# Performance work log

Hardware: AMD Instinct MI355X
Metric: run time of the kernel (lower is better)

The kernel has to match this reference:

```python
import jax, jax.numpy as jnp
import numpy as np

NUM_HEADS = 12


def setup_inputs() -> dict:
    key = jax.random.key(0)
    ks = jax.random.split(key, 5)
    B, N, D = 8, 1024, 768
    x = jax.random.normal(ks[0], (B, N, D), dtype=jnp.float32)
    w_qkv = jax.random.normal(ks[1], (D, 3 * D), dtype=jnp.float32) * (D ** -0.5)
    b_qkv = jax.random.normal(ks[2], (3 * D,), dtype=jnp.float32) * 0.02
    w_proj = jax.random.normal(ks[3], (D, D), dtype=jnp.float32) * (D ** -0.5)
    b_proj = jax.random.normal(ks[4], (D,), dtype=jnp.float32) * 0.02
    return {"x": x, "w_qkv": w_qkv, "b_qkv": b_qkv, "w_proj": w_proj, "b_proj": b_proj}


def reference(x, w_qkv, b_qkv, w_proj, b_proj):
    B, N, D = x.shape
    H = NUM_HEADS
    hd = D // H
    scale = hd ** -0.5
    qkv = x @ w_qkv + b_qkv                      # [B, N, 3D]
    qkv = qkv.reshape(B, N, 3, H, hd)
    q, k, v = jnp.moveaxis(qkv, 2, 0)            # each [B, N, H, hd]
    # scores: [B, H, N, N]
    scores = jnp.einsum("bqhd,bkhd->bhqk", q, k) * scale
    attn = jax.nn.softmax(scores, axis=-1)
    a = jnp.einsum("bhqk,bkhd->bqhd", attn, v)   # [B, N, H, hd]
    a = a.reshape(B, N, D)
    return a @ w_proj + b_proj
```

## Files before the change

### kernel.cpp

```cpp
#include <hip/hip_runtime.h>

#define B_ 8
#define N_ 1024
#define D_ 768
#define H_ 12
#define HD 64
#define M_ (B_*N_)

typedef short short8 __attribute__((ext_vector_type(8)));
typedef float f32x4 __attribute__((ext_vector_type(4)));
typedef float f32x16 __attribute__((ext_vector_type(16)));
typedef int int4v __attribute__((ext_vector_type(4)));

__device__ __forceinline__ unsigned short f2bf(float f) {
    union { float f; unsigned int u; } c; c.f = f;
    unsigned int u = c.u;
    unsigned int r = (u + 0x7fffu + ((u >> 16) & 1u)) >> 16;
    return (unsigned short)r;
}

__device__ __forceinline__ float exp2_hw(float x) {
    float r;
    asm("v_exp_f32 %0, %1" : "=v"(r) : "v"(x));
    return r;
}

__device__ __forceinline__ unsigned int cvtpk_bf16(float a, float b) {
    unsigned int r;
    asm("v_cvt_pk_bf16_f32 %0, %1, %2" : "=v"(r) : "v"(a), "v"(b));
    return r;
}

#define PLSWAP(a, b) asm volatile("v_permlane32_swap_b32 %0, %1" : "+&v"(a), "+&v"(b))

__device__ __forceinline__ short8 pack4(unsigned int a, unsigned int b,
                                        unsigned int c, unsigned int d) {
    union { int4v i; short8 s; } u;
    u.i = (int4v){(int)a, (int)b, (int)c, (int)d};
    return u.s;
}

__device__ __forceinline__ void gload16(const void* g, void* l) {
    __builtin_amdgcn_global_load_lds(
        (const __attribute__((address_space(1))) unsigned int*)g,
        (__attribute__((address_space(3))) unsigned int*)l, 16, 0, 0);
}


__global__ __launch_bounds__(256) void prep_kernel(
    const float* __restrict__ x, const float* __restrict__ wqkv,
    const float* __restrict__ wproj,
    unsigned short* __restrict__ xb, unsigned short* __restrict__ wqkvT,
    unsigned short* __restrict__ wprojT)
{
    int bid = blockIdx.x, tid = threadIdx.x;
    if (bid < 6144) {
        int i = bid * 256 + tid;
        float4 v = reinterpret_cast<const float4*>(x)[i];
        ushort4 o;
        o.x = f2bf(v.x); o.y = f2bf(v.y); o.z = f2bf(v.z); o.w = f2bf(v.w);
        reinterpret_cast<ushort4*>(xb)[i] = o;
    } else if (bid < 6144 + 6912) {
        int i = (bid - 6144) * 256 + tid;
        int r = i / 2304, c = i - r * 2304;
        wqkvT[c * 768 + r] = f2bf(wqkv[i]);
    } else {
        int i = (bid - 13056) * 256 + tid;
        int r = i / 768, c = i - r * 768;
        wprojT[c * 768 + r] = f2bf(wproj[i]);
    }
}


template<int MODE>
__global__ __launch_bounds__(256) void gemm_kernel(
    const unsigned short* __restrict__ A,
    const unsigned short* __restrict__ Bt,
    const float* __restrict__ bias,
    float* __restrict__ outf,
    unsigned short* __restrict__ qo,
    unsigned short* __restrict__ ko,
    unsigned short* __restrict__ vo,
    int Ndim, int K)
{
    __shared__ alignas(16) unsigned short As[3 * 4096];
    __shared__ alignas(16) unsigned short Bs[3 * 4096];

    int tid = threadIdx.x;
    int lane = tid & 63, w = tid >> 6;
    int wr = w >> 1, wc = w & 1;

    int nbx = Ndim >> 7;
    int nwg = gridDim.x;
    int cpx = nwg >> 3;
    int sbid = (blockIdx.x & 7) * cpx + (blockIdx.x >> 3);
    int bx = sbid % nbx, by = sbid / nbx;
    int m0 = by * 128, n0 = bx * 128;

    int lr = lane & 15, lk8 = (lane >> 4) * 8;
    int org = (lane >> 4) * 4;

    int srow = tid >> 2;
    int selem = (tid & 3) * 8;
    const unsigned short* gA = A + (size_t)(m0 + srow) * K + selem;
    const unsigned short* gB = Bt + (size_t)(n0 + srow) * K + selem;

    f32x4 acc[4][4] = {};

#define GSTAGE(buf, k0)                                                    \
    do {                                                                   \
        gload16(gA + (k0), As + (buf) * 4096 + w * 512);                   \
        gload16(gA + (size_t)64 * K + (k0), As + (buf) * 4096 + 2048 + w * 512);\
        gload16(gB + (k0), Bs + (buf) * 4096 + w * 512);                   \
        gload16(gB + (size_t)64 * K + (k0), Bs + (buf) * 4096 + 2048 + w * 512);\
    } while (0)

    GSTAGE(0, 0);
    GSTAGE(1, 32);
    asm volatile("s_waitcnt vmcnt(4)" ::: "memory");
    __builtin_amdgcn_s_barrier();
    __builtin_amdgcn_sched_barrier(0);

    int KT = K >> 5;
    int cur = 0;
    for (int kt = 0; kt < KT; ++kt) {
        int sb = cur + 2; if (sb >= 3) sb -= 3;
        if (kt + 2 < KT) GSTAGE(sb, (kt + 2) * 32);

        const unsigned short* Ab = As + cur * 4096;
        const unsigned short* Bb = Bs + cur * 4096;
        short8 af[4], bf[4];
        #pragma unroll
        for (int mi = 0; mi < 4; mi++)
            af[mi] = *reinterpret_cast<const short8*>(&Ab[(wr * 64 + mi * 16 + lr) * 32 + lk8]);
        #pragma unroll
        for (int ni = 0; ni < 4; ni++)
            bf[ni] = *reinterpret_cast<const short8*>(&Bb[(wc * 64 + ni * 16 + lr) * 32 + lk8]);
        #pragma unroll
        for (int mi = 0; mi < 4; mi++)
            #pragma unroll
            for (int ni = 0; ni < 4; ni++)
                acc[mi][ni] = (MODE == 1)
                    ? __builtin_amdgcn_mfma_f32_16x16x32_bf16(bf[ni], af[mi], acc[mi][ni], 0, 0, 0)
                    : __builtin_amdgcn_mfma_f32_16x16x32_bf16(af[mi], bf[ni], acc[mi][ni], 0, 0, 0);

        if (kt + 1 < KT) {
            if (kt + 2 < KT)
                asm volatile("s_waitcnt vmcnt(4)" ::: "memory");
            else
                asm volatile("s_waitcnt vmcnt(0)" ::: "memory");
            __builtin_amdgcn_s_barrier();
            __builtin_amdgcn_sched_barrier(0);
            cur = (cur == 2) ? 0 : cur + 1;
        }
    }
#undef GSTAGE

    if (MODE == 1) {
        int m = m0 + wr * 64 + lr;
        #pragma unroll
        for (int mi = 0; mi < 4; mi++) {
            int row = m + mi * 16;
            #pragma unroll
            for (int ni = 0; ni < 4; ni++) {
                int col = n0 + wc * 64 + ni * 16 + org;
                float4 bv = *reinterpret_cast<const float4*>(&bias[col]);
                float4 o;
                o.x = acc[mi][ni][0] + bv.x;
                o.y = acc[mi][ni][1] + bv.y;
                o.z = acc[mi][ni][2] + bv.z;
                o.w = acc[mi][ni][3] + bv.w;
                *reinterpret_cast<float4*>(&outf[(size_t)row * Ndim + col]) = o;
            }
        }
        return;
    }

    if (n0 >= 1536) {
        #pragma unroll
        for (int mi = 0; mi < 4; mi++) {
            int nn0g = m0 + wr * 64 + mi * 16 + org;
            int b = nn0g >> 10, nn = nn0g & 1023;
            #pragma unroll
            for (int ni = 0; ni < 4; ni++) {
                int colg = n0 + wc * 64 + ni * 16 + lr;
                int rem = colg - 1536;
                int h = rem >> 6, dd = rem & 63;
                float bv = bias[colg];
                unsigned long long u = 0;
                #pragma unroll
                for (int r = 0; r < 4; r++)
                    u |= (unsigned long long)f2bf(acc[mi][ni][r] + bv) << (16 * r);
                *reinterpret_cast<unsigned long long*>(
                    vo + ((size_t)(b * H_ + h) * HD + dd) * N_ + nn) = u;
            }
        }
    } else {
        int which = n0 / 768;
        unsigned short* dst = (which == 0) ? qo : ko;
        float fold = (which == 0) ? 0.125f * 1.44269504088896f : 1.0f;
        #pragma unroll
        for (int mi = 0; mi < 4; mi++) {
            #pragma unroll
            for (int ni = 0; ni < 4; ni++) {
                int col = n0 + wc * 64 + ni * 16 + lr;
                int rem = col - which * 768;
                int h = rem >> 6, dd = rem & 63;
                float bv = bias[col];
                #pragma unroll
                for (int r = 0; r < 4; r++) {
                    int row = m0 + wr * 64 + mi * 16 + org + r;
                    int b = row >> 10, nn = row & 1023;
                    dst[(((size_t)(b * H_ + h) * N_ + nn) * HD) + dd] =
                        f2bf((acc[mi][ni][r] + bv) * fold);
                }
            }
        }
    }
}


__global__ __launch_bounds__(256) void attn_kernel(
    const unsigned short* __restrict__ qg,
    const unsigned short* __restrict__ kg,
    const unsigned short* __restrict__ vtg,
    unsigned short* __restrict__ aout)
{
    __shared__ alignas(16) unsigned short Ks[2][4096];
    __shared__ alignas(16) unsigned short Vs[2][4096];

    int tid = threadIdx.x;
    int lane = tid & 63, w = tid >> 6;

    int bid = blockIdx.x;
    int xcd = bid & 7;
    int chunk = bid >> 3;
    int bh = xcd * 12 + (chunk % 12);
    int qblk = chunk / 12;
    int b = bh / H_, h = bh - b * H_;
    int q0w = qblk * 128 + w * 32;
    int l31 = lane & 31;
    int hi = lane >> 5;
    int swz = l31 & 7;

    const unsigned short* qp = qg + ((size_t)bh * N_ + q0w + l31) * HD + hi * 8;
    short8 qf[4];
    #pragma unroll
    for (int ds = 0; ds < 4; ds++)
        qf[ds] = *reinterpret_cast<const short8*>(qp + ds * 16);

    const unsigned short* kbh = kg + (size_t)bh * N_ * HD;
    const unsigned short* vtbh = vtg + (size_t)bh * HD * N_;

    int sr0 = tid >> 3;
    int sj0 = (tid & 7) ^ (sr0 & 7);
    int sr1 = sr0 + 32;
    int sj1 = (tid & 7) ^ (sr1 & 7);

    float m_run = -INFINITY, l_run = 0.f;
    f32x16 o0 = {}, o1 = {};

#define STAGE(buf, kv0)                                                        \
    do {                                                                       \
        gload16(kbh + (size_t)((kv0) + sr0) * HD + sj0 * 8, &Ks[buf][w * 512]);\
        gload16(kbh + (size_t)((kv0) + sr1) * HD + sj1 * 8, &Ks[buf][2048 + w * 512]);\
        gload16(vtbh + (size_t)sr0 * N_ + (kv0) + sj0 * 8, &Vs[buf][w * 512]); \
        gload16(vtbh + (size_t)sr1 * N_ + (kv0) + sj1 * 8, &Vs[buf][2048 + w * 512]);\
    } while (0)

    STAGE(0, 0);
    asm volatile("s_waitcnt vmcnt(0)" ::: "memory");
    __builtin_amdgcn_s_barrier();
    __builtin_amdgcn_sched_barrier(0);

    int cur = 0;
    for (int t = 0; t < 16; ++t) {
        if (t < 15) STAGE(cur ^ 1, (t + 1) * 64);

        const unsigned short* Ksb = Ks[cur];
        const unsigned short* Vsb = Vs[cur];

        f32x16 s0 = {}, s1 = {};
        #pragma unroll
        for (int ds = 0; ds < 4; ds++) {
            int pc = (ds * 2 + hi) ^ swz;
            short8 kf0 = *reinterpret_cast<const short8*>(&Ksb[(l31) * 64 + pc * 8]);
            short8 kf1 = *reinterpret_cast<const short8*>(&Ksb[(32 + l31) * 64 + pc * 8]);
            s0 = __builtin_amdgcn_mfma_f32_32x32x16_bf16(kf0, qf[ds], s0, 0, 0, 0);
            s1 = __builtin_amdgcn_mfma_f32_32x32x16_bf16(kf1, qf[ds], s1, 0, 0, 0);
        }

        float mx = s0[0];
        #pragma unroll
        for (int r = 1; r < 16; r++) mx = fmaxf(mx, s0[r]);
        #pragma unroll
        for (int r = 0; r < 16; r++) mx = fmaxf(mx, s1[r]);
        mx = fmaxf(mx, __shfl_xor(mx, 32, 64));

        if (__any(mx > m_run + 8.f)) {
            float mn = fmaxf(m_run, mx);
            float al = exp2_hw(m_run - mn);
            m_run = mn;
            l_run *= al;
            o0 *= al;
            o1 *= al;
        }

        float psum = 0.f;
        #pragma unroll
        for (int r = 0; r < 16; r++) { float p = exp2_hw(s0[r] - m_run); psum += p; s0[r] = p; }
        #pragma unroll
        for (int r = 0; r < 16; r++) { float p = exp2_hw(s1[r] - m_run); psum += p; s1[r] = p; }

        l_run += psum + __shfl_xor(psum, 32, 64);

        unsigned int c0[8], c1[8];
        #pragma unroll
        for (int i = 0; i < 8; i++) c0[i] = cvtpk_bf16(s0[2 * i], s0[2 * i + 1]);
        #pragma unroll
        for (int i = 0; i < 8; i++) c1[i] = cvtpk_bf16(s1[2 * i], s1[2 * i + 1]);
        PLSWAP(c0[0], c0[2]); PLSWAP(c0[1], c0[3]);
        PLSWAP(c0[4], c0[6]); PLSWAP(c0[5], c0[7]);
        PLSWAP(c1[0], c1[2]); PLSWAP(c1[1], c1[3]);
        PLSWAP(c1[4], c1[6]); PLSWAP(c1[5], c1[7]);
        short8 pa0 = pack4(c0[0], c0[1], c0[2], c0[3]);
        short8 pa1 = pack4(c0[4], c0[5], c0[6], c0[7]);
        short8 pa2 = pack4(c1[0], c1[1], c1[2], c1[3]);
        short8 pa3 = pack4(c1[4], c1[5], c1[6], c1[7]);

        #pragma unroll
        for (int ks = 0; ks < 4; ks++) {
            int pc = (ks * 2 + hi) ^ swz;
            short8 vf0 = *reinterpret_cast<const short8*>(&Vsb[(l31) * 64 + pc * 8]);
            short8 vf1 = *reinterpret_cast<const short8*>(&Vsb[(32 + l31) * 64 + pc * 8]);
            short8 pa = (ks == 0) ? pa0 : (ks == 1) ? pa1 : (ks == 2) ? pa2 : pa3;
            o0 = __builtin_amdgcn_mfma_f32_32x32x16_bf16(vf0, pa, o0, 0, 0, 0);
            o1 = __builtin_amdgcn_mfma_f32_32x32x16_bf16(vf1, pa, o1, 0, 0, 0);
        }

        if (t < 15) {
            asm volatile("s_waitcnt vmcnt(0)" ::: "memory");
            __builtin_amdgcn_s_barrier();
            __builtin_amdgcn_sched_barrier(0);
            cur ^= 1;
        }
    }
#undef STAGE

    float linv = 1.0f / l_run;
    unsigned short* op = aout + ((size_t)(b * N_ + q0w + l31)) * D_ + h * HD;
    #pragma unroll
    for (int rg = 0; rg < 4; rg++) {
        int dbase = 8 * rg + 4 * hi;
        unsigned long long u0 = 0, u1 = 0;
        #pragma unroll
        for (int k = 0; k < 4; k++) {
            u0 |= (unsigned long long)f2bf(o0[rg * 4 + k] * linv) << (16 * k);
            u1 |= (unsigned long long)f2bf(o1[rg * 4 + k] * linv) << (16 * k);
        }
        *reinterpret_cast<unsigned long long*>(op + dbase) = u0;
        *reinterpret_cast<unsigned long long*>(op + 32 + dbase) = u1;
    }
}


extern "C" void kernel_launch(void* const* d_in, const int* in_sizes, int n_in,
                              void* d_out, int out_size, void* d_ws, size_t ws_size,
                              hipStream_t stream) {
    const float* x      = (const float*)d_in[0];
    const float* w_qkv  = (const float*)d_in[1];
    const float* b_qkv  = (const float*)d_in[2];
    const float* w_proj = (const float*)d_in[3];
    const float* b_proj = (const float*)d_in[4];
    float* out = (float*)d_out;

    char* ws = (char*)d_ws;
    unsigned short* xb     = (unsigned short*)(ws + 0);
    unsigned short* wqkvT  = (unsigned short*)(ws + 12582912);
    unsigned short* wprojT = (unsigned short*)(ws + 16121856);
    unsigned short* qb     = (unsigned short*)(ws + 17301504);
    unsigned short* kb     = (unsigned short*)(ws + 29884416);
    unsigned short* vtb    = (unsigned short*)(ws + 42467328);
    unsigned short* aout   = xb;

    prep_kernel<<<15360, 256, 0, stream>>>(x, w_qkv, w_proj, xb, wqkvT, wprojT);

    gemm_kernel<0><<<1152, 256, 0, stream>>>(
        xb, wqkvT, b_qkv, nullptr, qb, kb, vtb, 3 * D_, D_);

    attn_kernel<<<768, 256, 0, stream>>>(qb, kb, vtb, aout);

    gemm_kernel<1><<<384, 256, 0, stream>>>(
        aout, wprojT, b_proj, out, nullptr, nullptr, nullptr, D_, D_);
}
```

Before: 145.8 us.

## Split QKV GEMM into 256x128 8-wave kernel with swizzled LDS and phased MFMA schedule

The QKV projection GEMM gets its own kernel. It uses 512-thread blocks with a 256x128 output tile, so each B tile in shared memory is reused across twice as many rows. Shared-memory reads now use an XOR swizzle to avoid bank conflicts. Each k-step is split into two halves, with the A and B prefetches interleaved between MFMA bursts and the MFMA bursts raised in priority through setprio. The output-projection GEMM keeps the old code as a separate kernel. The trade-offs are higher LDS use per block, extra barriers, and dropping the XCD-aware block remapping for the QKV GEMM.

```diff
diff --git a/kernel.cpp b/kernel.cpp
--- a/kernel.cpp
+++ b/kernel.cpp
@@ -72,109 +72,114 @@
 }
 
 
-template<int MODE>
-__global__ __launch_bounds__(256) void gemm_kernel(
+__global__ __launch_bounds__(512, 4) void gemm0_kernel(
     const unsigned short* __restrict__ A,
     const unsigned short* __restrict__ Bt,
     const float* __restrict__ bias,
-    float* __restrict__ outf,
     unsigned short* __restrict__ qo,
     unsigned short* __restrict__ ko,
-    unsigned short* __restrict__ vo,
-    int Ndim, int K)
+    unsigned short* __restrict__ vo)
 {
-    __shared__ alignas(16) unsigned short As[3 * 4096];
+    const int K = D_;
+    const int KT = K >> 5;
+    __shared__ alignas(16) unsigned short As[3 * 8192];
     __shared__ alignas(16) unsigned short Bs[3 * 4096];
 
     int tid = threadIdx.x;
     int lane = tid & 63, w = tid >> 6;
     int wr = w >> 1, wc = w & 1;
 
-    int nbx = Ndim >> 7;
-    int nwg = gridDim.x;
-    int cpx = nwg >> 3;
-    int sbid = (blockIdx.x & 7) * cpx + (blockIdx.x >> 3);
-    int bx = sbid % nbx, by = sbid / nbx;
-    int m0 = by * 128, n0 = bx * 128;
-
-    int lr = lane & 15, lk8 = (lane >> 4) * 8;
+    int m0 = blockIdx.y * 256, n0 = blockIdx.x * 128;
+
+    int lr = lane & 15;
+    int kc = lane >> 4;
     int org = (lane >> 4) * 4;
 
-    int srow = tid >> 2;
-    int selem = (tid & 3) * 8;
-    const unsigned short* gA = A + (size_t)(m0 + srow) * K + selem;
-    const unsigned short* gB = Bt + (size_t)(n0 + srow) * K + selem;
+    int srA = w * 16 + (lane >> 2);
+    int scA0 = (lane & 3) ^ (srA & 3);
+    int srA1 = 128 + srA;
+    int scA1 = (lane & 3) ^ (srA1 & 3);
+    const unsigned short* gA0 = A + (size_t)(m0 + srA) * K + scA0 * 8;
+    const unsigned short* gA1 = A + (size_t)(m0 + srA1) * K + scA1 * 8;
+    const unsigned short* gB0 = Bt + (size_t)(n0 + srA) * K + scA0 * 8;
 
     f32x4 acc[4][4] = {};
 
-#define GSTAGE(buf, k0)                                                    \
+#define STAGE_A(buf, k0)                                                   \
     do {                                                                   \
-        gload16(gA + (k0), As + (buf) * 4096 + w * 512);                   \
-        gload16(gA + (size_t)64 * K + (k0), As + (buf) * 4096 + 2048 + w * 512);\
-        gload16(gB + (k0), Bs + (buf) * 4096 + w * 512);                   \
-        gload16(gB + (size_t)64 * K + (k0), Bs + (buf) * 4096 + 2048 + w * 512);\
+        gload16(gA0 + (k0), As + (buf) * 8192 + w * 512);                  \
+        gload16(gA1 + (k0), As + (buf) * 8192 + 4096 + w * 512);           \
     } while (0)
-
-    GSTAGE(0, 0);
-    GSTAGE(1, 32);
-    asm volatile("s_waitcnt vmcnt(4)" ::: "memory");
+#define STAGE_B(buf, k0) gload16(gB0 + (k0), Bs + (buf) * 4096 + w * 512)
+
+    STAGE_A(0, 0); STAGE_B(0, 0);
+    STAGE_A(1, 32); STAGE_B(1, 32);
+    asm volatile("s_waitcnt vmcnt(3)" ::: "memory");
     __builtin_amdgcn_s_barrier();
     __builtin_amdgcn_sched_barrier(0);
 
-    int KT = K >> 5;
     int cur = 0;
     for (int kt = 0; kt < KT; ++kt) {
         int sb = cur + 2; if (sb >= 3) sb -= 3;
-        if (kt + 2 < KT) GSTAGE(sb, (kt + 2) * 32);
-
-        const unsigned short* Ab = As + cur * 4096;
+        bool pf = (kt + 2 < KT);
+        const unsigned short* Ab = As + cur * 8192;
         const unsigned short* Bb = Bs + cur * 4096;
-        short8 af[4], bf[4];
-        #pragma unroll
-        for (int mi = 0; mi < 4; mi++)
-            af[mi] = *reinterpret_cast<const short8*>(&Ab[(wr * 64 + mi * 16 + lr) * 32 + lk8]);
-        #pragma unroll
-        for (int ni = 0; ni < 4; ni++)
-            bf[ni] = *reinterpret_cast<const short8*>(&Bb[(wc * 64 + ni * 16 + lr) * 32 + lk8]);
-        #pragma unroll
-        for (int mi = 0; mi < 4; mi++)
-            #pragma unroll
-            for (int ni = 0; ni < 4; ni++)
-                acc[mi][ni] = (MODE == 1)
-                    ? __builtin_amdgcn_mfma_f32_16x16x32_bf16(bf[ni], af[mi], acc[mi][ni], 0, 0, 0)
-                    : __builtin_amdgcn_mfma_f32_16x16x32_bf16(af[mi], bf[ni], acc[mi][ni], 0, 0, 0);
-
-        if (kt + 1 < KT) {
-            if (kt + 2 < KT)
-                asm volatile("s_waitcnt vmcnt(4)" ::: "memory");
-            else
-                asm volatile("s_waitcnt vmcnt(0)" ::: "memory");
-            __builtin_amdgcn_s_barrier();
-            __builtin_amdgcn_sched_barrier(0);
-            cur = (cur == 2) ? 0 : cur + 1;
-        }
-    }
-#undef GSTAGE
-
-    if (MODE == 1) {
-        int m = m0 + wr * 64 + lr;
-        #pragma unroll
-        for (int mi = 0; mi < 4; mi++) {
-            int row = m + mi * 16;
+
+        short8 af0, af1, bf[4];
+        {
+            int r0 = wr * 64 + lr;
+            int r1 = wr * 64 + 16 + lr;
+            af0 = *reinterpret_cast<const short8*>(&Ab[r0 * 32 + (kc ^ (r0 & 3)) * 8]);
+            af1 = *reinterpret_cast<const short8*>(&Ab[r1 * 32 + (kc ^ (r1 & 3)) * 8]);
             #pragma unroll
             for (int ni = 0; ni < 4; ni++) {
-                int col = n0 + wc * 64 + ni * 16 + org;
-                float4 bv = *reinterpret_cast<const float4*>(&bias[col]);
-                float4 o;
-                o.x = acc[mi][ni][0] + bv.x;
-                o.y = acc[mi][ni][1] + bv.y;
-                o.z = acc[mi][ni][2] + bv.z;
-                o.w = acc[mi][ni][3] + bv.w;
-                *reinterpret_cast<float4*>(&outf[(size_t)row * Ndim + col]) = o;
+                int rb = wc * 64 + ni * 16 + lr;
+                bf[ni] = *reinterpret_cast<const short8*>(&Bb[rb * 32 + (kc ^ (rb & 3)) * 8]);
             }
         }
-        return;
-    }
+        if (pf) STAGE_A(sb, (kt + 2) * 32);
+        __builtin_amdgcn_s_barrier();
+        asm volatile("s_waitcnt lgkmcnt(0)" ::: "memory");
+        __builtin_amdgcn_sched_barrier(0);
+        __builtin_amdgcn_s_setprio(1);
+        #pragma unroll
+        for (int ni = 0; ni < 4; ni++) {
+            acc[0][ni] = __builtin_amdgcn_mfma_f32_16x16x32_bf16(af0, bf[ni], acc[0][ni], 0, 0, 0);
+            acc[1][ni] = __builtin_amdgcn_mfma_f32_16x16x32_bf16(af1, bf[ni], acc[1][ni], 0, 0, 0);
+        }
+        __builtin_amdgcn_s_setprio(0);
+        __builtin_amdgcn_s_barrier();
+        __builtin_amdgcn_sched_barrier(0);
+
+        short8 af2, af3;
+        {
+            int r2 = wr * 64 + 32 + lr;
+            int r3 = wr * 64 + 48 + lr;
+            af2 = *reinterpret_cast<const short8*>(&Ab[r2 * 32 + (kc ^ (r2 & 3)) * 8]);
+            af3 = *reinterpret_cast<const short8*>(&Ab[r3 * 32 + (kc ^ (r3 & 3)) * 8]);
+        }
+        if (pf) STAGE_B(sb, (kt + 2) * 32);
+        __builtin_amdgcn_s_barrier();
+        asm volatile("s_waitcnt lgkmcnt(0)" ::: "memory");
+        __builtin_amdgcn_sched_barrier(0);
+        __builtin_amdgcn_s_setprio(1);
+        #pragma unroll
+        for (int ni = 0; ni < 4; ni++) {
+            acc[2][ni] = __builtin_amdgcn_mfma_f32_16x16x32_bf16(af2, bf[ni], acc[2][ni], 0, 0, 0);
+            acc[3][ni] = __builtin_amdgcn_mfma_f32_16x16x32_bf16(af3, bf[ni], acc[3][ni], 0, 0, 0);
+        }
+        __builtin_amdgcn_s_setprio(0);
+        if (kt + 1 < KT) {
+            if (pf) asm volatile("s_waitcnt vmcnt(3)" ::: "memory");
+            else    asm volatile("s_waitcnt vmcnt(0)" ::: "memory");
+        }
+        __builtin_amdgcn_s_barrier();
+        __builtin_amdgcn_sched_barrier(0);
+
+        cur = (cur == 2) ? 0 : cur + 1;
+    }
+#undef STAGE_A
+#undef STAGE_B
 
     if (n0 >= 1536) {
         #pragma unroll
@@ -220,6 +225,103 @@
 }
 
 
+__global__ __launch_bounds__(256) void gemm1_kernel(
+    const unsigned short* __restrict__ A,
+    const unsigned short* __restrict__ Bt,
+    const float* __restrict__ bias,
+    float* __restrict__ outf,
+    int Ndim, int K)
+{
+    __shared__ alignas(16) unsigned short As[3 * 4096];
+    __shared__ alignas(16) unsigned short Bs[3 * 4096];
+
+    int tid = threadIdx.x;
+    int lane = tid & 63, w = tid >> 6;
+    int wr = w >> 1, wc = w & 1;
+
+    int nbx = Ndim >> 7;
+    int nwg = gridDim.x;
+    int cpx = nwg >> 3;
+    int sbid = (blockIdx.x & 7) * cpx + (blockIdx.x >> 3);
+    int bx = sbid % nbx, by = sbid / nbx;
+    int m0 = by * 128, n0 = bx * 128;
+
+    int lr = lane & 15, lk8 = (lane >> 4) * 8;
+    int org = (lane >> 4) * 4;
+
+    int srow = tid >> 2;
+    int selem = (tid & 3) * 8;
+    const unsigned short* gA = A + (size_t)(m0 + srow) * K + selem;
+    const unsigned short* gB = Bt + (size_t)(n0 + srow) * K + selem;
+
+    f32x4 acc[4][4] = {};
+
+#define GSTAGE(buf, k0)                                                    \
+    do {                                                                   \
+        gload16(gA + (k0), As + (buf) * 4096 + w * 512);                   \
+        gload16(gA + (size_t)64 * K + (k0), As + (buf) * 4096 + 2048 + w * 512);\
+        gload16(gB + (k0), Bs + (buf) * 4096 + w * 512);                   \
+        gload16(gB + (size_t)64 * K + (k0), Bs + (buf) * 4096 + 2048 + w * 512);\
+    } while (0)
+
+    GSTAGE(0, 0);
+    GSTAGE(1, 32);
+    asm volatile("s_waitcnt vmcnt(4)" ::: "memory");
+    __builtin_amdgcn_s_barrier();
+    __builtin_amdgcn_sched_barrier(0);
+
+    int KT = K >> 5;
+    int cur = 0;
+    for (int kt = 0; kt < KT; ++kt) {
+        int sb = cur + 2; if (sb >= 3) sb -= 3;
+        if (kt + 2 < KT) GSTAGE(sb, (kt + 2) * 32);
+
+        const unsigned short* Ab = As + cur * 4096;
+        const unsigned short* Bb = Bs + cur * 4096;
+        short8 af[4], bf[4];
+        #pragma unroll
+        for (int mi = 0; mi < 4; mi++)
+            af[mi] = *reinterpret_cast<const short8*>(&Ab[(wr * 64 + mi * 16 + lr) * 32 + lk8]);
+        #pragma unroll
+        for (int ni = 0; ni < 4; ni++)
+            bf[ni] = *reinterpret_cast<const short8*>(&Bb[(wc * 64 + ni * 16 + lr) * 32 + lk8]);
+        #pragma unroll
+        for (int mi = 0; mi < 4; mi++)
+            #pragma unroll
+            for (int ni = 0; ni < 4; ni++)
+                acc[mi][ni] = __builtin_amdgcn_mfma_f32_16x16x32_bf16(bf[ni], af[mi], acc[mi][ni], 0, 0, 0);
+
+        if (kt + 1 < KT) {
+            if (kt + 2 < KT)
+                asm volatile("s_waitcnt vmcnt(4)" ::: "memory");
+            else
+                asm volatile("s_waitcnt vmcnt(0)" ::: "memory");
+            __builtin_amdgcn_s_barrier();
+            __builtin_amdgcn_sched_barrier(0);
+            cur = (cur == 2) ? 0 : cur + 1;
+        }
+    }
+#undef GSTAGE
+
+    int m = m0 + wr * 64 + lr;
+    #pragma unroll
+    for (int mi = 0; mi < 4; mi++) {
+        int row = m + mi * 16;
+        #pragma unroll
+        for (int ni = 0; ni < 4; ni++) {
+            int col = n0 + wc * 64 + ni * 16 + org;
+            float4 bv = *reinterpret_cast<const float4*>(&bias[col]);
+            float4 o;
+            o.x = acc[mi][ni][0] + bv.x;
+            o.y = acc[mi][ni][1] + bv.y;
+            o.z = acc[mi][ni][2] + bv.z;
+            o.w = acc[mi][ni][3] + bv.w;
+            *reinterpret_cast<float4*>(&outf[(size_t)row * Ndim + col]) = o;
+        }
+    }
+}
+
+
 __global__ __launch_bounds__(256) void attn_kernel(
     const unsigned short* __restrict__ qg,
     const unsigned short* __restrict__ kg,
@@ -385,11 +487,11 @@
 
     prep_kernel<<<15360, 256, 0, stream>>>(x, w_qkv, w_proj, xb, wqkvT, wprojT);
 
-    gemm_kernel<0><<<1152, 256, 0, stream>>>(
-        xb, wqkvT, b_qkv, nullptr, qb, kb, vtb, 3 * D_, D_);
+    gemm0_kernel<<<dim3(18, 32), 512, 0, stream>>>(
+        xb, wqkvT, b_qkv, qb, kb, vtb);
 
     attn_kernel<<<768, 256, 0, stream>>>(qb, kb, vtb, aout);
 
-    gemm_kernel<1><<<384, 256, 0, stream>>>(
-        aout, wprojT, b_proj, out, nullptr, nullptr, nullptr, D_, D_);
-}
+    gemm1_kernel<<<384, 256, 0, stream>>>(
+        aout, wprojT, b_proj, out, D_, D_);
+}
```

Result: faster. 134.8 us (-7.6%).
